# Kernel tuning notes

Hardware: AMD Instinct MI355X
Metric: run time of the kernel (lower is better)

Reference implementation:

```python
import jax, jax.numpy as jnp
import numpy as np

T, B, IN, OUT, N_MODULES, K = 2048, 8, 1024, 1024, 16, 2


def setup_inputs() -> dict:
    key = jax.random.key(0)
    k1, k2, k3 = jax.random.split(key, 3)
    x = jax.random.normal(k1, (T, B, IN), dtype=jnp.float32)          # time-major input
    selection = jax.random.randint(k2, (B, K), 0, N_MODULES, dtype=jnp.int32)
    # kaiming-uniform-ish scale for [n_modules, out, in] weight
    bound = 1.0 / np.sqrt(IN)
    weight = jax.random.uniform(k3, (N_MODULES, OUT, IN), dtype=jnp.float32,
                                minval=-bound, maxval=bound)
    return {"x": x, "selection": selection, "weight": weight}


def reference(x, selection, weight):
    # Faithful to ModularLinear.forward with time_major=True, sum_outputs=False, bias=None.
    # Original computes o = x @ all-expert weights -> [B, n_modules, T, out], then for each
    # selection column i gathers o[b, selection[b, i]] and concats on the last dim.
    # Equivalent math: gather the selected expert weights per (batch, slot) and do one GEMM.
    # x: [T, B, in]; selection: [B, K]; weight: [n_modules, out, in]
    w_sel = weight[selection]                              # [B, K, out, in]
    o = jnp.einsum('tbi,bkoi->tbko', x, w_sel)             # [T, B, K, out]
    t, b, k, d = o.shape
    return o.reshape(t, b, k * d)                          # [T, B, K*out]
```

## Files before the change

kernel.cpp:

```cpp
#include <hip/hip_runtime.h>

#define T_DIM   2048
#define B_DIM   8
#define IN_DIM  1024
#define OUT_DIM 1024
#define NMOD    16
#define KSLOT   2

#define BM 256
#define BN 256
#define BK 64
#define NT (IN_DIM / BK)
#define AS_STRIDE (B_DIM * IN_DIM)

typedef __bf16 bf16x8 __attribute__((ext_vector_type(8)));
typedef float  f32x4  __attribute__((ext_vector_type(4)));
typedef unsigned short ushort8 __attribute__((ext_vector_type(8)));

typedef const __attribute__((address_space(1))) void* gptr_t;
typedef __attribute__((address_space(3))) void* lptr_t;

__device__ __forceinline__ void async_load16(const void* gp, void* lp) {
  __builtin_amdgcn_global_load_lds((gptr_t)gp, (lptr_t)lp, 16, 0, 0);
}

__device__ __forceinline__ unsigned short f2bf_rne(float f) {
  unsigned int u = __float_as_uint(f);
  u += 0x7fffu + ((u >> 16) & 1u);
  return (unsigned short)(u >> 16);
}

__global__ __launch_bounds__(256) void convert_bf16(
    const float* __restrict__ x, const float* __restrict__ w,
    unsigned short* __restrict__ xb, unsigned short* __restrict__ wb) {
  const long tid = (long)blockIdx.x * blockDim.x + threadIdx.x;
  const long XV = (long)T_DIM * B_DIM * IN_DIM / 8;
  const float4* src;
  unsigned short* dst;
  long v;
  if (tid < XV) { v = tid;      src = (const float4*)x; dst = xb; }
  else          { v = tid - XV; src = (const float4*)w; dst = wb; }
  float4 a = src[2 * v];
  float4 c = src[2 * v + 1];
  ushort8 o;
  o[0] = f2bf_rne(a.x); o[1] = f2bf_rne(a.y); o[2] = f2bf_rne(a.z); o[3] = f2bf_rne(a.w);
  o[4] = f2bf_rne(c.x); o[5] = f2bf_rne(c.y); o[6] = f2bf_rne(c.z); o[7] = f2bf_rne(c.w);
  *(ushort8*)(dst + v * 8) = o;
}

#define S_BARRIER()  asm volatile("s_barrier" ::: "memory")
#define WAIT_LGKM0() asm volatile("s_waitcnt lgkmcnt(0)" ::: "memory")

__global__ __launch_bounds__(512, 2) void gemm_mod(
    const unsigned short* __restrict__ xb, const unsigned short* __restrict__ wb,
    const int* __restrict__ sel, float* __restrict__ out) {
  __shared__ alignas(16) unsigned short As[2][BM * BK];
  __shared__ alignas(16) unsigned short Bs[2][BN * BK];

  const int nt = blockIdx.x;
  const int mt = blockIdx.y;
  const int bk = blockIdx.z;
  const int b  = bk >> 1;
  const int ks = bk & 1;
  const int expert = sel[bk];

  const unsigned short* Ab = xb + ((long)mt * BM * B_DIM + b) * IN_DIM;
  const unsigned short* Bb = wb + ((long)expert * OUT_DIM + (long)nt * BN) * IN_DIM;

  const int tid  = threadIdx.x;
  const int lane = tid & 63;
  const int lm   = lane & 15;
  const int kg   = lane >> 4;
  const int rsw  = lm & 7;
  const int w    = tid >> 6;
  const int wm   = (w >> 2) * 128;
  const int wn   = (w & 3) * 64;

  int aoff[2][2], alds[2][2], boff[2][2], blds[2][2];
  #pragma unroll
  for (int j = 0; j < 2; ++j) {
    #pragma unroll
    for (int h = 0; h < 2; ++h) {
      const int c = j * 1024 + h * 512 + tid;
      const int r = c >> 3, g = (c & 7) ^ (r & 7);
      aoff[j][h] = r * AS_STRIDE + g * 8;
      alds[j][h] = c * 8;
      const int cc = j * 512 + tid;
      const int c2 = (cc >> 8) * 512 + h * 256 + (cc & 255);
      const int r2 = c2 >> 3, g2 = (c2 & 7) ^ (r2 & 7);
      boff[j][h] = r2 * IN_DIM + g2 * 8;
      blds[j][h] = c2 * 8;
    }
  }

#define STAGE_A(d, kt, h) do { \
    async_load16(Ab + aoff[0][h] + (kt) * BK, &As[d][alds[0][h]]); \
    async_load16(Ab + aoff[1][h] + (kt) * BK, &As[d][alds[1][h]]); } while (0)
#define STAGE_B(d, kt, h) do { \
    async_load16(Bb + boff[0][h] + (kt) * BK, &Bs[d][blds[0][h]]); \
    async_load16(Bb + boff[1][h] + (kt) * BK, &Bs[d][blds[1][h]]); } while (0)
#define LDA(d, row, gs) (*(const bf16x8*)&As[d][((((row) << 3) + ((gs) ^ rsw)) << 3)])
#define LDB(d, row, gs) (*(const bf16x8*)&Bs[d][((((row) << 3) + ((gs) ^ rsw)) << 3)])

  f32x4 acc[8][4];
  const f32x4 z = {0.f, 0.f, 0.f, 0.f};
  #pragma unroll
  for (int i = 0; i < 8; ++i)
    #pragma unroll
    for (int j = 0; j < 4; ++j) acc[i][j] = z;

  STAGE_A(0, 0, 0);
  STAGE_B(0, 0, 1);
  STAGE_A(0, 0, 1);
  STAGE_B(0, 0, 0);
  STAGE_A(1, 1, 0);
  STAGE_B(1, 1, 1);
  STAGE_A(1, 1, 1);
  asm volatile("s_waitcnt vmcnt(6)" ::: "memory");
  S_BARRIER();

  for (int t = 0; t < NT; ++t) {
    const int cur = t & 1;
    const int nxt = cur ^ 1;
    bf16x8 af[4][2], b0[2][2], b1[2][2];

    #pragma unroll
    for (int mi = 0; mi < 4; ++mi)
      #pragma unroll
      for (int kst = 0; kst < 2; ++kst)
        af[mi][kst] = LDA(cur, wm + mi * 16 + lm, kst * 4 + kg);
    #pragma unroll
    for (int ni = 0; ni < 2; ++ni)
      #pragma unroll
      for (int kst = 0; kst < 2; ++kst)
        b0[ni][kst] = LDB(cur, wn + ni * 16 + lm, kst * 4 + kg);
    if (t + 1 < NT) STAGE_B(nxt, t + 1, 0);
    S_BARRIER();
    WAIT_LGKM0();
    __builtin_amdgcn_s_setprio(1);
    #pragma unroll
    for (int mi = 0; mi < 4; ++mi)
      #pragma unroll
      for (int ni = 0; ni < 2; ++ni)
        #pragma unroll
        for (int kst = 0; kst < 2; ++kst)
          acc[mi][ni] = __builtin_amdgcn_mfma_f32_16x16x32_bf16(
              af[mi][kst], b0[ni][kst], acc[mi][ni], 0, 0, 0);
    __builtin_amdgcn_s_setprio(0);
    S_BARRIER();

    #pragma unroll
    for (int nj = 0; nj < 2; ++nj)
      #pragma unroll
      for (int kst = 0; kst < 2; ++kst)
        b1[nj][kst] = LDB(cur, wn + (2 + nj) * 16 + lm, kst * 4 + kg);
    if (t + 2 < NT) STAGE_A(cur, t + 2, 0);
    S_BARRIER();
    WAIT_LGKM0();
    __builtin_amdgcn_s_setprio(1);
    #pragma unroll
    for (int mi = 0; mi < 4; ++mi)
      #pragma unroll
      for (int nj = 0; nj < 2; ++nj)
        #pragma unroll
        for (int kst = 0; kst < 2; ++kst)
          acc[mi][2 + nj] = __builtin_amdgcn_mfma_f32_16x16x32_bf16(
              af[mi][kst], b1[nj][kst], acc[mi][2 + nj], 0, 0, 0);
    __builtin_amdgcn_s_setprio(0);
    S_BARRIER();

    #pragma unroll
    for (int mi = 0; mi < 4; ++mi)
      #pragma unroll
      for (int kst = 0; kst < 2; ++kst)
        af[mi][kst] = LDA(cur, wm + 64 + mi * 16 + lm, kst * 4 + kg);
    if (t + 2 < NT) STAGE_B(cur, t + 2, 1);
    S_BARRIER();
    WAIT_LGKM0();
    __builtin_amdgcn_s_setprio(1);
    #pragma unroll
    for (int mi = 0; mi < 4; ++mi)
      #pragma unroll
      for (int nj = 0; nj < 2; ++nj)
        #pragma unroll
        for (int kst = 0; kst < 2; ++kst)
          acc[4 + mi][2 + nj] = __builtin_amdgcn_mfma_f32_16x16x32_bf16(
              af[mi][kst], b1[nj][kst], acc[4 + mi][2 + nj], 0, 0, 0);
    __builtin_amdgcn_s_setprio(0);
    S_BARRIER();

    if (t + 2 < NT) STAGE_A(cur, t + 2, 1);
    __builtin_amdgcn_s_setprio(1);
    #pragma unroll
    for (int mi = 0; mi < 4; ++mi)
      #pragma unroll
      for (int ni = 0; ni < 2; ++ni)
        #pragma unroll
        for (int kst = 0; kst < 2; ++kst)
          acc[4 + mi][ni] = __builtin_amdgcn_mfma_f32_16x16x32_bf16(
              af[mi][kst], b0[ni][kst], acc[4 + mi][ni], 0, 0, 0);
    __builtin_amdgcn_s_setprio(0);
    if (t < NT - 2) {
      asm volatile("s_waitcnt vmcnt(6)" ::: "memory");
    } else {
      asm volatile("s_waitcnt vmcnt(0)" ::: "memory");
    }
    S_BARRIER();
  }

  const int row0 = mt * BM + wm + kg * 4;
  const int col0 = nt * BN + wn + lm;
  #pragma unroll
  for (int mi = 0; mi < 8; ++mi) {
    #pragma unroll
    for (int r = 0; r < 4; ++r) {
      const int t_row = row0 + mi * 16 + r;
      float* po = out + (long)t_row * (B_DIM * KSLOT * OUT_DIM)
                      + b * (KSLOT * OUT_DIM) + ks * OUT_DIM + col0;
      #pragma unroll
      for (int ni = 0; ni < 4; ++ni)
        po[ni * 16] = acc[mi][ni][r];
    }
  }
#undef STAGE_A
#undef STAGE_B
#undef LDA
#undef LDB
}

extern "C" void kernel_launch(void* const* d_in, const int* in_sizes, int n_in,
                              void* d_out, int out_size, void* d_ws, size_t ws_size,
                              hipStream_t stream) {
  const float* x   = (const float*)d_in[0];
  const int*   sel = (const int*)d_in[1];
  const float* w   = (const float*)d_in[2];
  float* out = (float*)d_out;

  unsigned short* xb = (unsigned short*)d_ws;
  unsigned short* wb = xb + (long)T_DIM * B_DIM * IN_DIM;

  const long total_vecs =
      ((long)T_DIM * B_DIM * IN_DIM + (long)NMOD * OUT_DIM * IN_DIM) / 8;
  convert_bf16<<<dim3((unsigned)((total_vecs + 255) / 256)), 256, 0, stream>>>(x, w, xb, wb);

  dim3 ggrid(OUT_DIM / BN, T_DIM / BM, B_DIM * KSLOT);
  gemm_mod<<<ggrid, 512, 0, stream>>>(xb, wb, sel, out);
}
```

Before: 300.1 us.

## Fuse both expert slots into one persistent block pipeline per batch

Each block now computes both K-slot outputs for a batch row tile sequentially, running a single continuous double-buffered pipeline over 2*NT k-steps and storing the first tile mid-loop. This removes one pipeline prologue and drain per pair of tiles and halves the grid to 512 blocks, so the next expert's loads overlap the tail of the first. The cost is that grid parallelism halves (512 blocks at 2 per CU on 256 CUs is about one wave) and the mid-loop store may stall the pipeline.

```diff
diff --git a/kernel.cpp b/kernel.cpp
--- a/kernel.cpp
+++ b/kernel.cpp
@@ -11,6 +11,7 @@
 #define BN 256
 #define BK 64
 #define NT (IN_DIM / BK)
+#define NU (2 * NT)
 #define AS_STRIDE (B_DIM * IN_DIM)
 
 typedef __bf16 bf16x8 __attribute__((ext_vector_type(8)));
@@ -59,13 +60,13 @@
 
   const int nt = blockIdx.x;
   const int mt = blockIdx.y;
-  const int bk = blockIdx.z;
-  const int b  = bk >> 1;
-  const int ks = bk & 1;
-  const int expert = sel[bk];
-
-  const unsigned short* Ab = xb + ((long)mt * BM * B_DIM + b) * IN_DIM;
-  const unsigned short* Bb = wb + ((long)expert * OUT_DIM + (long)nt * BN) * IN_DIM;
+  const int b  = blockIdx.z;
+  const int e0 = sel[2 * b];
+  const int e1 = sel[2 * b + 1];
+
+  const unsigned short* Ab  = xb + ((long)mt * BM * B_DIM + b) * IN_DIM;
+  const unsigned short* Bw0 = wb + ((long)e0 * OUT_DIM + (long)nt * BN) * IN_DIM;
+  const unsigned short* Bw1 = wb + ((long)e1 * OUT_DIM + (long)nt * BN) * IN_DIM;
 
   const int tid  = threadIdx.x;
   const int lane = tid & 63;
@@ -93,12 +94,14 @@
     }
   }
 
-#define STAGE_A(d, kt, h) do { \
-    async_load16(Ab + aoff[0][h] + (kt) * BK, &As[d][alds[0][h]]); \
-    async_load16(Ab + aoff[1][h] + (kt) * BK, &As[d][alds[1][h]]); } while (0)
-#define STAGE_B(d, kt, h) do { \
-    async_load16(Bb + boff[0][h] + (kt) * BK, &Bs[d][blds[0][h]]); \
-    async_load16(Bb + boff[1][h] + (kt) * BK, &Bs[d][blds[1][h]]); } while (0)
+#define KOF(v) (((v) & (NT - 1)) * BK)
+#define STAGE_A(d, v, h) do { \
+    async_load16(Ab + aoff[0][h] + KOF(v), &As[d][alds[0][h]]); \
+    async_load16(Ab + aoff[1][h] + KOF(v), &As[d][alds[1][h]]); } while (0)
+#define STAGE_B(d, v, h) do { \
+    const unsigned short* _bs = ((v) < NT ? Bw0 : Bw1); \
+    async_load16(_bs + boff[0][h] + KOF(v), &Bs[d][blds[0][h]]); \
+    async_load16(_bs + boff[1][h] + KOF(v), &Bs[d][blds[1][h]]); } while (0)
 #define LDA(d, row, gs) (*(const bf16x8*)&As[d][((((row) << 3) + ((gs) ^ rsw)) << 3)])
 #define LDB(d, row, gs) (*(const bf16x8*)&Bs[d][((((row) << 3) + ((gs) ^ rsw)) << 3)])
 
@@ -108,6 +111,20 @@
   for (int i = 0; i < 8; ++i)
     #pragma unroll
     for (int j = 0; j < 4; ++j) acc[i][j] = z;
+
+  const int row0 = mt * BM + wm + kg * 4;
+  const int col0 = nt * BN + wn + lm;
+#define STORE_TILE(ksl) do { \
+    _Pragma("unroll") \
+    for (int mi = 0; mi < 8; ++mi) { \
+      _Pragma("unroll") \
+      for (int r = 0; r < 4; ++r) { \
+        const int tr = row0 + mi * 16 + r; \
+        float* po = out + (long)tr * (B_DIM * KSLOT * OUT_DIM) \
+                        + b * (KSLOT * OUT_DIM) + (ksl) * OUT_DIM + col0; \
+        _Pragma("unroll") \
+        for (int ni = 0; ni < 4; ++ni) po[ni * 16] = acc[mi][ni][r]; \
+      } } } while (0)
 
   STAGE_A(0, 0, 0);
   STAGE_B(0, 0, 1);
@@ -119,8 +136,16 @@
   asm volatile("s_waitcnt vmcnt(6)" ::: "memory");
   S_BARRIER();
 
-  for (int t = 0; t < NT; ++t) {
-    const int cur = t & 1;
+  #pragma unroll 2
+  for (int u = 0; u < NU; ++u) {
+    if (u == NT) {
+      STORE_TILE(0);
+      #pragma unroll
+      for (int i = 0; i < 8; ++i)
+        #pragma unroll
+        for (int j = 0; j < 4; ++j) acc[i][j] = z;
+    }
+    const int cur = u & 1;
     const int nxt = cur ^ 1;
     bf16x8 af[4][2], b0[2][2], b1[2][2];
 
@@ -134,7 +159,7 @@
       #pragma unroll
       for (int kst = 0; kst < 2; ++kst)
         b0[ni][kst] = LDB(cur, wn + ni * 16 + lm, kst * 4 + kg);
-    if (t + 1 < NT) STAGE_B(nxt, t + 1, 0);
+    if (u + 1 < NU) STAGE_B(nxt, u + 1, 0);
     S_BARRIER();
     WAIT_LGKM0();
     __builtin_amdgcn_s_setprio(1);
@@ -154,7 +179,7 @@
       #pragma unroll
       for (int kst = 0; kst < 2; ++kst)
         b1[nj][kst] = LDB(cur, wn + (2 + nj) * 16 + lm, kst * 4 + kg);
-    if (t + 2 < NT) STAGE_A(cur, t + 2, 0);
+    if (u + 2 < NU) STAGE_A(cur, u + 2, 0);
     S_BARRIER();
     WAIT_LGKM0();
     __builtin_amdgcn_s_setprio(1);
@@ -174,7 +199,7 @@
       #pragma unroll
       for (int kst = 0; kst < 2; ++kst)
         af[mi][kst] = LDA(cur, wm + 64 + mi * 16 + lm, kst * 4 + kg);
-    if (t + 2 < NT) STAGE_B(cur, t + 2, 1);
+    if (u + 2 < NU) STAGE_B(cur, u + 2, 1);
     S_BARRIER();
     WAIT_LGKM0();
     __builtin_amdgcn_s_setprio(1);
@@ -189,7 +214,7 @@
     __builtin_amdgcn_s_setprio(0);
     S_BARRIER();
 
-    if (t + 2 < NT) STAGE_A(cur, t + 2, 1);
+    if (u + 2 < NU) STAGE_A(cur, u + 2, 1);
     __builtin_amdgcn_s_setprio(1);
     #pragma unroll
     for (int mi = 0; mi < 4; ++mi)
@@ -200,7 +225,7 @@
           acc[4 + mi][ni] = __builtin_amdgcn_mfma_f32_16x16x32_bf16(
               af[mi][kst], b0[ni][kst], acc[4 + mi][ni], 0, 0, 0);
     __builtin_amdgcn_s_setprio(0);
-    if (t < NT - 2) {
+    if (u < NU - 2) {
       asm volatile("s_waitcnt vmcnt(6)" ::: "memory");
     } else {
       asm volatile("s_waitcnt vmcnt(0)" ::: "memory");
@@ -208,24 +233,14 @@
     S_BARRIER();
   }
 
-  const int row0 = mt * BM + wm + kg * 4;
-  const int col0 = nt * BN + wn + lm;
-  #pragma unroll
-  for (int mi = 0; mi < 8; ++mi) {
-    #pragma unroll
-    for (int r = 0; r < 4; ++r) {
-      const int t_row = row0 + mi * 16 + r;
-      float* po = out + (long)t_row * (B_DIM * KSLOT * OUT_DIM)
-                      + b * (KSLOT * OUT_DIM) + ks * OUT_DIM + col0;
-      #pragma unroll
-      for (int ni = 0; ni < 4; ++ni)
-        po[ni * 16] = acc[mi][ni][r];
-    }
-  }
+  STORE_TILE(1);
+
 #undef STAGE_A
 #undef STAGE_B
+#undef STORE_TILE
 #undef LDA
 #undef LDB
+#undef KOF
 }
 
 extern "C" void kernel_launch(void* const* d_in, const int* in_sizes, int n_in,
@@ -243,6 +258,6 @@
       ((long)T_DIM * B_DIM * IN_DIM + (long)NMOD * OUT_DIM * IN_DIM) / 8;
   convert_bf16<<<dim3((unsigned)((total_vecs + 255) / 256)), 256, 0, stream>>>(x, w, xb, wb);
 
-  dim3 ggrid(OUT_DIM / BN, T_DIM / BM, B_DIM * KSLOT);
+  dim3 ggrid(OUT_DIM / BN, T_DIM / BM, B_DIM);
   gemm_mod<<<ggrid, 512, 0, stream>>>(xb, wb, sel, out);
 }
```

Result: slower. 357.5 us (+19.1%).
